# Performance work log

Measured on AMD Instinct MI355X. Metric: run time of the kernel, lower is better.

Reference implementation:

```python
import jax, jax.numpy as jnp
import numpy as np

B, W, CBLK, C, H, L, VOCAB = 8, 512, 24, 512, 8, 2, 256
HD = C // H


def _ln(x, g, b, eps=1e-5):
    m = x.mean(-1, keepdims=True)
    v = ((x - m) ** 2).mean(-1, keepdims=True)
    return (x - m) * jax.lax.rsqrt(v + eps) * g + b


def _causal_attn(q, k, v):
    # q,k,v: [..., T, hd]; causal softmax attention, scale 1/sqrt(hd)
    T = q.shape[-2]
    scale = 1.0 / (q.shape[-1] ** 0.5)
    s = jnp.einsum('...qd,...kd->...qk', q, k) * scale
    mask = jnp.tril(jnp.ones((T, T), dtype=bool))
    s = jnp.where(mask, s, jnp.finfo(s.dtype).min)
    return jnp.einsum('...qk,...kd->...qd', jax.nn.softmax(s, axis=-1), v)


def _mha_char(seq, w_qkv, last_ix):
    # seq: [B,W,c,C]; per-word causal char attention, then gather row last_ix
    b, w, c, _ = seq.shape
    q, k, v = jnp.split(seq @ w_qkv, 3, axis=-1)
    sh = lambda t: t.reshape(b, w, c, H, HD).transpose(0, 1, 3, 2, 4)
    o = _causal_attn(sh(q), sh(k), sh(v))          # [B,W,H,c,hd]
    o = o.transpose(0, 1, 3, 2, 4).reshape(b, w, c, C)
    return jnp.take_along_axis(o, last_ix[:, :, None, None], axis=2)[:, :, 0, :]


def _mha_word(x, w_qkv, w_proj):
    b, w, _ = x.shape
    q, k, v = jnp.split(x @ w_qkv, 3, axis=-1)
    sh = lambda t: t.reshape(b, w, H, HD).transpose(0, 2, 1, 3)
    o = _causal_attn(sh(q), sh(k), sh(v))
    o = o.transpose(0, 2, 1, 3).reshape(b, w, C)
    return o @ w_proj


def setup_inputs() -> dict:
    key = jax.random.key(0)
    ks = jax.random.split(key, 16)
    # ragged word lengths in [1, CBLK]; mask = ones then zeros (as produced by pad())
    lengths = jax.random.randint(ks[0], (B, W), 1, CBLK + 1)
    attention_mask = (jnp.arange(CBLK)[None, None, :] < lengths[:, :, None]).astype(jnp.int32)
    x = jax.random.randint(ks[1], (B, W, CBLK), 0, VOCAB).astype(jnp.int32)
    std = 0.02
    res_std = std * (2 * L) ** -0.5  # res_flag init scaling
    n = lambda k, s, sd=std: sd * jax.random.normal(k, s, dtype=jnp.float32)
    return dict(
        x=x, attention_mask=attention_mask,
        cte=n(ks[2], (VOCAB, C)), cpe=n(ks[3], (CBLK, C)), wpe=n(ks[4], (W, C)),
        ln1_g=jnp.ones((L, C)), ln1_b=jnp.zeros((L, C)),
        ln2_g=jnp.ones((L, C)), ln2_b=jnp.zeros((L, C)),
        ln3_g=jnp.ones((L, C)), ln3_b=jnp.zeros((L, C)),
        cattn_w=n(ks[5], (L, C, 3 * C)), cattn_proj=n(ks[6], (L, C, C)),
        wattn_w=n(ks[7], (L, C, 3 * C)), wattn_proj=n(ks[8], (L, C, C), res_std),
        mlp_fc=n(ks[9], (L, C, 4 * C)), mlp_proj=n(ks[10], (L, 4 * C, C), res_std),
        proj_w=n(ks[11], (C, CBLK * C)), lm_head_w=n(ks[12], (C, VOCAB)),
    )


def reference(x, attention_mask, cte, cpe, wpe, ln1_g, ln1_b, ln2_g, ln2_b, ln3_g, ln3_b,
              cattn_w, cattn_proj, wattn_w, wattn_proj, mlp_fc, mlp_proj, proj_w, lm_head_w):
    last_ix = attention_mask.sum(axis=2) - 1           # [B,W], last real char per word
    state = cte[x] + cpe[None, None, :, :]             # [B,W,c,C]
    context = None                                     # current_conv.context/pad, vectorized
    for l in range(L):
        if l == 0:
            # first_time: operate on full padded char sequences, cache ln_1 output
            hln = _ln(state, ln1_g[l], ln1_b[l])       # [B,W,c,C]
            context = hln
            seq = hln
        else:
            # splice the new word vector into position last_ix of the cached context
            hln = _ln(state, ln1_g[l], ln1_b[l])       # [B,W,C]
            repl = jnp.arange(CBLK)[None, None, :] == last_ix[:, :, None]
            seq = jnp.where(repl[..., None], hln[:, :, None, :], context)
        o = _mha_char(seq, cattn_w[l], last_ix)        # [B,W,C]
        if l == 0:
            o = o + wpe[None, :, :]                    # word pos emb added only first_time
        state = o @ cattn_proj[l]                      # note: no residual around c_attn
        state = state + _mha_word(_ln(state, ln2_g[l], ln2_b[l]), wattn_w[l], wattn_proj[l])
        hm = _ln(state, ln3_g[l], ln3_b[l])
        state = state + jax.nn.gelu(hm @ mlp_fc[l], approximate=False) @ mlp_proj[l]
    y = (state @ proj_w).reshape(B, W, CBLK, C)
    return y @ lm_head_w                               # logits [B,W,CBLK,VOCAB]
```

## Files before the change

kernel.cpp:

```cpp
#include <hip/hip_runtime.h>
#include <hip/hip_bf16.h>
#include <math.h>


namespace {

constexpr int Bn = 8, Wn = 512, CB = 24, Cd = 512, Hn = 8, Lln = 2, Vn = 256, HDn = 64;
constexpr int BW = Bn * Wn;
constexpr int C3 = 3 * Cd;
constexpr int FF = 4 * Cd;
constexpr int NROW = BW * CB;

typedef unsigned short u16;
typedef short short8 __attribute__((ext_vector_type(8)));
typedef float f32x4 __attribute__((ext_vector_type(4)));
typedef __attribute__((address_space(1))) void gvoid_t;
typedef __attribute__((address_space(3))) void lvoid_t;

__device__ __forceinline__ u16 f2bu(float f) {
  __hip_bfloat16 h = __float2bfloat16(f);
  return __builtin_bit_cast(u16, h);
}
__device__ __forceinline__ float bu2f(u16 u) {
  return __bfloat162float(__builtin_bit_cast(__hip_bfloat16, u));
}
__device__ __forceinline__ float geluf(float x) {
  return 0.5f * x * (1.0f + erff(x * 0.7071067811865475f));
}
__device__ __forceinline__ void gl16(const void* g, void* l) {
  __builtin_amdgcn_global_load_lds((gvoid_t*)g, (lvoid_t*)l, 16, 0, 0);
}

__global__ void k_lastix(const int* __restrict__ mask, int* __restrict__ lastix) {
  int i = blockIdx.x * 256 + threadIdx.x;
  if (i < BW) {
    int s = 0;
#pragma unroll
    for (int j = 0; j < CB; ++j) s += mask[i * CB + j];
    lastix[i] = s - 1;
  }
}

__device__ __forceinline__ void f2b8(const float* __restrict__ s, u16* __restrict__ d) {
  float4 a = *(const float4*)s;
  float4 b = *(const float4*)(s + 4);
  union { uint4 u; u16 h[8]; } pk;
  pk.h[0] = f2bu(a.x); pk.h[1] = f2bu(a.y); pk.h[2] = f2bu(a.z); pk.h[3] = f2bu(a.w);
  pk.h[4] = f2bu(b.x); pk.h[5] = f2bu(b.y); pk.h[6] = f2bu(b.z); pk.h[7] = f2bu(b.w);
  *(uint4*)d = pk.u;
}

__device__ __forceinline__ void wT_tile(const float* __restrict__ src, u16* __restrict__ dst,
                                        int K, int N, int n0, int k0,
                                        u16 T[64][72], int tid) {
  int kl = tid >> 2, nc = (tid & 3) * 16;
  const float* s = src + (long)(k0 + kl) * N + n0 + nc;
#pragma unroll
  for (int u = 0; u < 4; ++u) {
    float4 f = *(const float4*)(s + u * 4);
    T[nc + u * 4 + 0][kl] = f2bu(f.x);
    T[nc + u * 4 + 1][kl] = f2bu(f.y);
    T[nc + u * 4 + 2][kl] = f2bu(f.z);
    T[nc + u * 4 + 3][kl] = f2bu(f.w);
  }
  __syncthreads();
  int nl = tid >> 2, kc = (tid & 3) * 16;
  u16* d = dst + (long)(n0 + nl) * K + k0 + kc;
  *(uint4*)d = *(uint4*)&T[nl][kc];
  *(uint4*)(d + 8) = *(uint4*)&T[nl][kc + 8];
}

__global__ __launch_bounds__(256) void k_prep(
    const float* __restrict__ proj_w, u16* __restrict__ projwb,
    const float* __restrict__ cattn_w, u16* __restrict__ wcb,
    const float* __restrict__ lm_head, u16* __restrict__ lmhT,
    const float* __restrict__ cattn_proj, const float* __restrict__ wattn_w,
    const float* __restrict__ wattn_proj, const float* __restrict__ mlp_fc,
    const float* __restrict__ mlp_proj, u16* __restrict__ wT) {
  __shared__ u16 T[64][72];
  int b = blockIdx.x, tid = threadIdx.x;
  if (b < 3072) { long i = ((long)b * 256 + tid) * 8; f2b8(proj_w + i, projwb + i); return; }
  b -= 3072;
  if (b < 768) { long i = ((long)b * 256 + tid) * 8; f2b8(cattn_w + i, wcb + i); return; }
  b -= 768;
  if (b < 32) { wT_tile(lm_head, lmhT, Cd, Vn, (b & 3) * 64, (b >> 2) * 64, T, tid); return; }
  b -= 32;
  int l = b >> 10, r = b & 1023;
  size_t lw = (size_t)(2 * C3 * Cd + 2 * Cd * Cd + 2 * FF * Cd);
  u16* bl = wT + l * lw;
  const float* src; u16* dst; int K, N, nt;
  if (r < 192)      { src = cattn_w + (size_t)l * Cd * C3;    dst = bl;                              K = Cd; N = C3; nt = 24; }
  else if (r < 256) { src = cattn_proj + (size_t)l * Cd * Cd; dst = bl + C3 * Cd;                    K = Cd; N = Cd; nt = 8;  r -= 192; }
  else if (r < 448) { src = wattn_w + (size_t)l * Cd * C3;    dst = bl + C3 * Cd + Cd * Cd;          K = Cd; N = C3; nt = 24; r -= 256; }
  else if (r < 512) { src = wattn_proj + (size_t)l * Cd * Cd; dst = bl + 2 * C3 * Cd + Cd * Cd;      K = Cd; N = Cd; nt = 8;  r -= 448; }
  else if (r < 768) { src = mlp_fc + (size_t)l * Cd * FF;     dst = bl + 2 * C3 * Cd + 2 * Cd * Cd;  K = Cd; N = FF; nt = 32; r -= 512; }
  else              { src = mlp_proj + (size_t)l * FF * Cd;   dst = bl + 2 * C3 * Cd + 2 * Cd * Cd + FF * Cd; K = FF; N = Cd; nt = 8; r -= 768; }
  wT_tile(src, dst, K, N, (r % nt) * 64, (r / nt) * 64, T, tid);
}

__global__ __launch_bounds__(64) void k_embed_ln(
    const int* __restrict__ x, const float* __restrict__ cte, const float* __restrict__ cpe,
    const float* __restrict__ g, const float* __restrict__ b,
    const int* __restrict__ lastix, u16* __restrict__ ctx, u16* __restrict__ qin) {
  int r = blockIdx.x;
  int bw = r / CB, ch = r - bw * CB;
  int li = lastix[bw];
  if (ch > li) return;
  int tok = x[r];
  const float* e = cte + (long)tok * Cd;
  const float* pe = cpe + (long)ch * Cd;
  int lane = threadIdx.x;
  float v[8];
  float s = 0.f, sq = 0.f;
#pragma unroll
  for (int u = 0; u < 2; ++u) {
    float4 a = *(const float4*)(e + u * 256 + lane * 4);
    float4 p4 = *(const float4*)(pe + u * 256 + lane * 4);
    v[u * 4 + 0] = a.x + p4.x; v[u * 4 + 1] = a.y + p4.y;
    v[u * 4 + 2] = a.z + p4.z; v[u * 4 + 3] = a.w + p4.w;
  }
#pragma unroll
  for (int u = 0; u < 8; ++u) { s += v[u]; sq += v[u] * v[u]; }
#pragma unroll
  for (int m = 32; m; m >>= 1) { s += __shfl_xor(s, m); sq += __shfl_xor(sq, m); }
  float mean = s * (1.0f / Cd);
  float var = sq * (1.0f / Cd) - mean * mean;
  float rs = rsqrtf(var + 1e-5f);
  u16* o = ctx + (long)r * Cd;
  u16* oq = qin + (long)bw * Cd;
  int isLast = (ch == li);
#pragma unroll
  for (int u = 0; u < 2; ++u) {
    int c0 = u * 256 + lane * 4;
    float4 g4 = *(const float4*)(g + c0);
    float4 b4 = *(const float4*)(b + c0);
    float o0 = (v[u * 4 + 0] - mean) * rs * g4.x + b4.x;
    float o1 = (v[u * 4 + 1] - mean) * rs * g4.y + b4.y;
    float o2 = (v[u * 4 + 2] - mean) * rs * g4.z + b4.z;
    float o3 = (v[u * 4 + 3] - mean) * rs * g4.w + b4.w;
    uint2 w;
    w.x = (unsigned)f2bu(o0) | ((unsigned)f2bu(o1) << 16);
    w.y = (unsigned)f2bu(o2) | ((unsigned)f2bu(o3) << 16);
    *(uint2*)(o + c0) = w;
    if (isLast) *(uint2*)(oq + c0) = w;
  }
}

__global__ __launch_bounds__(64) void k_ln(
    const float* __restrict__ X, u16* __restrict__ Y,
    const float* __restrict__ g, const float* __restrict__ b) {
  long r = blockIdx.x;
  const float* xr = X + r * Cd;
  int lane = threadIdx.x;
  float v[8];
  float s = 0.f, sq = 0.f;
#pragma unroll
  for (int u = 0; u < 2; ++u) {
    float4 a = *(const float4*)(xr + u * 256 + lane * 4);
    v[u * 4 + 0] = a.x; v[u * 4 + 1] = a.y; v[u * 4 + 2] = a.z; v[u * 4 + 3] = a.w;
  }
#pragma unroll
  for (int u = 0; u < 8; ++u) { s += v[u]; sq += v[u] * v[u]; }
#pragma unroll
  for (int m = 32; m; m >>= 1) { s += __shfl_xor(s, m); sq += __shfl_xor(sq, m); }
  float mean = s * (1.0f / Cd);
  float var = sq * (1.0f / Cd) - mean * mean;
  float rs = rsqrtf(var + 1e-5f);
  u16* o = Y + r * Cd;
#pragma unroll
  for (int u = 0; u < 2; ++u) {
    int c0 = u * 256 + lane * 4;
    float4 g4 = *(const float4*)(g + c0);
    float4 b4 = *(const float4*)(b + c0);
    float o0 = (v[u * 4 + 0] - mean) * rs * g4.x + b4.x;
    float o1 = (v[u * 4 + 1] - mean) * rs * g4.y + b4.y;
    float o2 = (v[u * 4 + 2] - mean) * rs * g4.z + b4.z;
    float o3 = (v[u * 4 + 3] - mean) * rs * g4.w + b4.w;
    uint2 w;
    w.x = (unsigned)f2bu(o0) | ((unsigned)f2bu(o1) << 16);
    w.y = (unsigned)f2bu(o2) | ((unsigned)f2bu(o3) << 16);
    *(uint2*)(o + c0) = w;
  }
}

template <int BM, int BN, int EPI, int OUTBF>
__global__ __launch_bounds__(256) void k_mgemm(
    const u16* __restrict__ A, int lda, long sA1, long sA2,
    const u16* __restrict__ Bt, int ldb, long sB1, long sB2,
    void* __restrict__ Cv, int ldc, long sC1, long sC2,
    const float* __restrict__ R, u16* __restrict__ D2,
    const float* __restrict__ PL, const u16* __restrict__ VL,
    const float* __restrict__ WP, int K, int zdiv) {
  constexpr int WM = BM / 2;
  constexpr int WN = BN / 2;
  constexpr int FM = WM / 16, FN = WN / 16;
  __shared__ u16 As[BM * 32];
  __shared__ u16 Bs[BN * 32];
  long m0 = (long)blockIdx.y * BM, n0 = (long)blockIdx.x * BN;
  int z = blockIdx.z;
  int z1 = z / zdiv, z2 = z - z1 * zdiv;
  A += z1 * sA1 + z2 * sA2;
  Bt += z1 * sB1 + z2 * sB2;
  long coff = z1 * sC1 + z2 * sC2;
  int tid = threadIdx.x;
  int wid = tid >> 6, lane = tid & 63;
  int wr = wid >> 1, wc = wid & 1;

  const int srow = tid >> 2, skk = (tid & 3) * 8;
  const u16* Ald[BM / 64];
  const u16* Bld[BN / 64];
#pragma unroll
  for (int i = 0; i < BM / 64; ++i) Ald[i] = A + (m0 + srow + i * 64) * (long)lda + skk;
#pragma unroll
  for (int i = 0; i < BN / 64; ++i) Bld[i] = Bt + (n0 + srow + i * 64) * (long)ldb + skk;

  f32x4 acc[FM][FN] = {};
  const int fr = lane & 15, kg = lane >> 4;

  for (int k0 = 0; k0 < K; k0 += 32) {
#pragma unroll
    for (int i = 0; i < BM / 64; ++i) gl16(Ald[i] + k0, &As[(tid + i * 256) * 8]);
#pragma unroll
    for (int i = 0; i < BN / 64; ++i) gl16(Bld[i] + k0, &Bs[(tid + i * 256) * 8]);
    __syncthreads();
    short8 af[FM], bf[FN];
#pragma unroll
    for (int m = 0; m < FM; ++m)
      af[m] = *(const short8*)&As[(wr * WM + m * 16 + fr) * 32 + kg * 8];
#pragma unroll
    for (int n = 0; n < FN; ++n)
      bf[n] = *(const short8*)&Bs[(wc * WN + n * 16 + fr) * 32 + kg * 8];
#pragma unroll
    for (int m = 0; m < FM; ++m)
#pragma unroll
      for (int n = 0; n < FN; ++n)
        acc[m][n] = __builtin_amdgcn_mfma_f32_16x16x32_bf16(af[m], bf[n], acc[m][n], 0, 0, 0);
    __syncthreads();
  }
  int ccol = lane & 15, crow4 = (lane >> 4) * 4;
#pragma unroll
  for (int m = 0; m < FM; ++m)
#pragma unroll
    for (int n = 0; n < FN; ++n)
#pragma unroll
      for (int q = 0; q < 4; ++q) {
        long gr = m0 + wr * WM + m * 16 + crow4 + q;
        long gc = n0 + wc * WN + n * 16 + ccol;
        float v = acc[m][n][q];
        long idx = gr * (long)ldc + gc + coff;
        if (EPI == 1 || EPI == 3) v += R[idx];
        if (EPI == 2) v = geluf(v);
        if (EPI == 4) {
          v += PL[gr * 8 + z2] * bu2f(VL[gr * (long)C3 + 2 * Cd + z2 * 64 + gc]);
          if (WP) v += WP[(long)(gr & (Wn - 1)) * Cd + z2 * 64 + gc];
        }
        if (EPI == 3) {
          ((float*)Cv)[idx] = v;
          D2[idx] = f2bu(v);
        } else if (OUTBF) {
          ((u16*)Cv)[idx] = f2bu(v);
        } else {
          ((float*)Cv)[idx] = v;
        }
      }
}

__global__ __launch_bounds__(256) void k_cattn2(
    const u16* __restrict__ ctx, const u16* __restrict__ qtil,
    const u16* __restrict__ qkvc, const int* __restrict__ lastix,
    u16* __restrict__ U, float* __restrict__ plast) {
  constexpr int CS = 520;
  int gw = blockIdx.x;
  int li = lastix[gw];
  __shared__ u16 ctxs[CB - 1][CS];
  __shared__ float spf[4][Hn][32];
  __shared__ float sp[Hn][CB];
  int tid = threadIdx.x;
  for (int u = tid; u < li * 64; u += 256) {
    int row = u >> 6, c = (u & 63) * 8;
    *(uint4*)&ctxs[row][c] = *(const uint4*)(ctx + ((long)(gw * CB + row)) * Cd + c);
  }
  __syncthreads();
  int w = tid >> 6, lane = tid & 63;
  int fr = lane & 15, kg = lane >> 4;
  {
    const u16* qbase = qtil + (long)gw * 4096 + (fr & 7) * 512 + w * 128 + kg * 8;
    int r0 = fr;
    int r1 = 16 + fr; if (r1 > CB - 2) r1 = CB - 2;
    f32x4 acc0 = {}, acc1 = {};
#pragma unroll
    for (int kk = 0; kk < 4; ++kk) {
      short8 af = *(const short8*)(qbase + kk * 32);
      short8 b0 = *(const short8*)&ctxs[r0][w * 128 + kk * 32 + kg * 8];
      short8 b1 = *(const short8*)&ctxs[r1][w * 128 + kk * 32 + kg * 8];
      acc0 = __builtin_amdgcn_mfma_f32_16x16x32_bf16(af, b0, acc0, 0, 0, 0);
      acc1 = __builtin_amdgcn_mfma_f32_16x16x32_bf16(af, b1, acc1, 0, 0, 0);
    }
    if (lane < 32) {
      int jj = lane & 15;
#pragma unroll
      for (int q = 0; q < 4; ++q) {
        int h = (lane >> 4) * 4 + q;
        spf[w][h][jj] = acc0[q];
        spf[w][h][16 + jj] = acc1[q];
      }
    }
  }
  __syncthreads();
  {
    int h = tid >> 5, j = tid & 31;
    if (j < CB)
      sp[h][j] = (spf[0][h][j] + spf[1][h][j] + spf[2][h][j] + spf[3][h][j]) * 0.125f;
  }
  __syncthreads();
  if (tid < 8) {
    const u16* qq = qkvc + (long)gw * C3 + tid * 64;
    const u16* kk = qq + Cd;
    float s = 0.f;
#pragma unroll
    for (int u = 0; u < 64; ++u) s += bu2f(qq[u]) * bu2f(kk[u]);
    sp[tid][li] = s * 0.125f;
  }
  __syncthreads();
  if (tid < 8) {
    float m = -3.4e38f;
    for (int jj = 0; jj <= li; ++jj) m = fmaxf(m, sp[tid][jj]);
    float s = 0.f;
    for (int jj = 0; jj <= li; ++jj) { float e = expf(sp[tid][jj] - m); sp[tid][jj] = e; s += e; }
    float inv = 1.0f / s;
    for (int jj = 0; jj <= li; ++jj) sp[tid][jj] *= inv;
    plast[gw * 8 + tid] = sp[tid][li];
  }
  __syncthreads();
  int h = tid >> 5, d0 = (tid & 31) * 16;
  float uacc[16];
#pragma unroll
  for (int i = 0; i < 16; ++i) uacc[i] = 0.f;
  for (int jj = 0; jj < li; ++jj) {
    float p = sp[h][jj];
    const u16* cv = &ctxs[jj][d0];
#pragma unroll
    for (int i = 0; i < 16; ++i) uacc[i] += p * bu2f(cv[i]);
  }
  union { uint4 q[2]; u16 hh[16]; } pk;
#pragma unroll
  for (int i = 0; i < 16; ++i) pk.hh[i] = f2bu(uacc[i]);
  u16* d = U + (long)gw * 4096 + h * 512 + d0;
  *(uint4*)d = pk.q[0];
  *(uint4*)(d + 8) = pk.q[1];
}

__global__ __launch_bounds__(256) void k_fattn(
    const u16* __restrict__ qkv, u16* __restrict__ ao) {
  constexpr int ST = 68;
  __shared__ u16 Ks[64 * ST];
  __shared__ u16 Vs[64 * ST];
  __shared__ u16 Ps[4][16 * ST];
  int qt = blockIdx.x;
  int z  = blockIdx.y;
  int b = z >> 3, h = z & 7;
  int tid = threadIdx.x;
  int w = tid >> 6, lane = tid & 63;
  int fr = lane & 15, kg = lane >> 4;

  short8 qf[2];
  {
    const u16* qp = qkv + ((long)(b * Wn + qt * 64 + w * 16 + fr)) * C3 + h * 64 + kg * 8;
    qf[0] = *(const short8*)qp;
    qf[1] = *(const short8*)(qp + 32);
  }
  f32x4 oacc[4] = {};
  float mrow[4], lrow[4];
#pragma unroll
  for (int q = 0; q < 4; ++q) { mrow[q] = -3.4e38f; lrow[q] = 0.f; }

  for (int kt = 0; kt <= qt; ++kt) {
    __syncthreads();
    {
      int r = tid >> 2, c = (tid & 3) * 16;
      const u16* kp = qkv + ((long)(b * Wn + kt * 64 + r)) * C3 + Cd + h * 64 + c;
      *(uint4*)&Ks[r * ST + c] = *(const uint4*)kp;
      *(uint4*)&Ks[r * ST + c + 8] = *(const uint4*)(kp + 8);
      const u16* vp = kp + Cd;
      uint4 v0 = *(const uint4*)vp;
      uint4 v1 = *(const uint4*)(vp + 8);
      const u16* e0 = (const u16*)&v0;
      const u16* e1 = (const u16*)&v1;
#pragma unroll
      for (int u = 0; u < 8; ++u) Vs[(c + u) * ST + r] = e0[u];
#pragma unroll
      for (int u = 0; u < 8; ++u) Vs[(c + 8 + u) * ST + r] = e1[u];
    }
    __syncthreads();
    f32x4 s[4];
#pragma unroll
    for (int n = 0; n < 4; ++n) {
      short8 kf0 = *(const short8*)&Ks[(n * 16 + fr) * ST + kg * 8];
      short8 kf1 = *(const short8*)&Ks[(n * 16 + fr) * ST + kg * 8 + 32];
      f32x4 a = {};
      a = __builtin_amdgcn_mfma_f32_16x16x32_bf16(qf[0], kf0, a, 0, 0, 0);
      a = __builtin_amdgcn_mfma_f32_16x16x32_bf16(qf[1], kf1, a, 0, 0, 0);
      s[n] = a;
    }
    int irow0 = qt * 64 + w * 16 + kg * 4;
#pragma unroll
    for (int n = 0; n < 4; ++n) {
      int jcol = kt * 64 + n * 16 + fr;
#pragma unroll
      for (int q = 0; q < 4; ++q) {
        float v = s[n][q] * 0.125f;
        s[n][q] = (jcol > irow0 + q) ? -3.4e38f : v;
      }
    }
    float sf[4];
#pragma unroll
    for (int q = 0; q < 4; ++q) {
      float mm = fmaxf(fmaxf(s[0][q], s[1][q]), fmaxf(s[2][q], s[3][q]));
      mm = fmaxf(mm, __shfl_xor(mm, 1));
      mm = fmaxf(mm, __shfl_xor(mm, 2));
      mm = fmaxf(mm, __shfl_xor(mm, 4));
      mm = fmaxf(mm, __shfl_xor(mm, 8));
      float mnew = fmaxf(mrow[q], mm);
      sf[q] = expf(mrow[q] - mnew);
      mrow[q] = mnew;
    }
    float ls[4] = {0.f, 0.f, 0.f, 0.f};
#pragma unroll
    for (int n = 0; n < 4; ++n) {
#pragma unroll
      for (int q = 0; q < 4; ++q) {
        float p = expf(s[n][q] - mrow[q]);
        u16 pb = f2bu(p);
        ls[q] += bu2f(pb);
        Ps[w][(kg * 4 + q) * ST + n * 16 + fr] = pb;
      }
    }
#pragma unroll
    for (int q = 0; q < 4; ++q) {
      float l = ls[q];
      l += __shfl_xor(l, 1); l += __shfl_xor(l, 2);
      l += __shfl_xor(l, 4); l += __shfl_xor(l, 8);
      lrow[q] = lrow[q] * sf[q] + l;
#pragma unroll
      for (int n = 0; n < 4; ++n) oacc[n][q] *= sf[q];
    }
    asm volatile("s_waitcnt lgkmcnt(0)" ::: "memory");
    short8 pa0 = *(const short8*)&Ps[w][fr * ST + kg * 8];
    short8 pa1 = *(const short8*)&Ps[w][fr * ST + kg * 8 + 32];
#pragma unroll
    for (int n = 0; n < 4; ++n) {
      short8 vf0 = *(const short8*)&Vs[(n * 16 + fr) * ST + kg * 8];
      short8 vf1 = *(const short8*)&Vs[(n * 16 + fr) * ST + kg * 8 + 32];
      oacc[n] = __builtin_amdgcn_mfma_f32_16x16x32_bf16(pa0, vf0, oacc[n], 0, 0, 0);
      oacc[n] = __builtin_amdgcn_mfma_f32_16x16x32_bf16(pa1, vf1, oacc[n], 0, 0, 0);
    }
  }
  int orow = b * Wn + qt * 64 + w * 16 + kg * 4;
#pragma unroll
  for (int q = 0; q < 4; ++q) {
    float inv = 1.0f / lrow[q];
#pragma unroll
    for (int n = 0; n < 4; ++n)
      ao[(long)(orow + q) * Cd + h * 64 + n * 16 + fr] = f2bu(oacc[n][q] * inv);
  }
}

template <int BM, int BN, int EPI, int OUTBF>
static inline void mgemm(hipStream_t st,
    const u16* A, int lda, long sA1, long sA2,
    const u16* Bt, int ldb, long sB1, long sB2,
    void* C, int ldc, long sC1, long sC2,
    const float* R, int M, int N, int K, int nz, int zdiv,
    u16* D2 = nullptr, const float* PL = nullptr, const u16* VL = nullptr,
    const float* WP = nullptr) {
  dim3 g(N / BN, (M + BM - 1) / BM, nz);
  hipLaunchKernelGGL((k_mgemm<BM, BN, EPI, OUTBF>), g, dim3(256), 0, st,
                     A, lda, sA1, sA2, Bt, ldb, sB1, sB2, C, ldc, sC1, sC2,
                     R ? R : (const float*)C, D2, PL, VL, WP, K, zdiv);
}

}

extern "C" void kernel_launch(void* const* d_in, const int* in_sizes, int n_in,
                              void* d_out, int out_size, void* d_ws, size_t ws_size,
                              hipStream_t stream) {
  (void)in_sizes; (void)n_in; (void)out_size; (void)ws_size;
  const int*   x          = (const int*)d_in[0];
  const int*   amask      = (const int*)d_in[1];
  const float* cte        = (const float*)d_in[2];
  const float* cpe        = (const float*)d_in[3];
  const float* wpe        = (const float*)d_in[4];
  const float* ln1g       = (const float*)d_in[5];
  const float* ln1b       = (const float*)d_in[6];
  const float* ln2g       = (const float*)d_in[7];
  const float* ln2b       = (const float*)d_in[8];
  const float* ln3g       = (const float*)d_in[9];
  const float* ln3b       = (const float*)d_in[10];
  const float* cattn_w    = (const float*)d_in[11];
  const float* cattn_proj = (const float*)d_in[12];
  const float* wattn_w    = (const float*)d_in[13];
  const float* wattn_proj = (const float*)d_in[14];
  const float* mlp_fc     = (const float*)d_in[15];
  const float* mlp_proj   = (const float*)d_in[16];
  const float* proj_w     = (const float*)d_in[17];
  const float* lm_head    = (const float*)d_in[18];
  float* out = (float*)d_out;

  char* base = (char*)d_ws;
  size_t off = 0;
  auto alloc = [&](size_t bytes) -> char* {
    char* r = base + off;
    off += (bytes + 255) & ~(size_t)255;
    return r;
  };
  int*   lastix = (int*)alloc((size_t)BW * 4);
  float* plast  = (float*)alloc((size_t)BW * 8 * 4);
  u16*   ctx    = (u16*)alloc((size_t)NROW * Cd * 2);
  char*  big    = alloc((size_t)105 * 1024 * 1024);
  u16*   kvq    = (u16*)alloc((size_t)BW * C3 * 2);
  u16*   qin    = (u16*)alloc((size_t)BW * Cd * 2);
  float* state  = (float*)alloc((size_t)BW * Cd * 4);
  u16*   stateb = (u16*)alloc((size_t)BW * Cd * 2);
  u16*   hln    = (u16*)alloc((size_t)BW * Cd * 2);
  u16*   ao     = (u16*)alloc((size_t)BW * Cd * 2);
  u16*   wT     = (u16*)alloc((size_t)2 * (2 * C3 * Cd + 2 * Cd * Cd + 2 * FF * Cd) * 2);
  u16*   wcb    = (u16*)alloc((size_t)2 * Cd * C3 * 2);
  u16*   projwb = (u16*)alloc((size_t)Cd * CB * Cd * 2);
  u16*   lmhT   = (u16*)alloc((size_t)Vn * Cd * 2);

  u16*   U     = (u16*)big;
  u16*   qtil  = (u16*)(big + (size_t)35651584);
  u16*   mlph  = (u16*)big;
  u16*   combT = (u16*)big;

  size_t lw = (size_t)(2 * C3 * Cd + 2 * Cd * Cd + 2 * FF * Cd);
  auto cwT    = [&](int l) { return wT + l * lw; };
  auto cprojT = [&](int l) { return wT + l * lw + C3 * Cd; };
  auto wwT    = [&](int l) { return wT + l * lw + C3 * Cd + Cd * Cd; };
  auto wprojT = [&](int l) { return wT + l * lw + 2 * C3 * Cd + Cd * Cd; };
  auto fcT    = [&](int l) { return wT + l * lw + 2 * C3 * Cd + 2 * Cd * Cd; };
  auto mprojT = [&](int l) { return wT + l * lw + 2 * C3 * Cd + 2 * Cd * Cd + FF * Cd; };

  hipLaunchKernelGGL(k_lastix, dim3(16), dim3(256), 0, stream, amask, lastix);
  hipLaunchKernelGGL(k_prep, dim3(5920), dim3(256), 0, stream,
                     proj_w, projwb, cattn_w, wcb, lm_head, lmhT,
                     cattn_proj, wattn_w, wattn_proj, mlp_fc, mlp_proj, wT);
  hipLaunchKernelGGL(k_embed_ln, dim3(NROW), dim3(64), 0, stream,
                     x, cte, cpe, ln1g, ln1b, lastix, ctx, qin);

  for (int l = 0; l < Lln; ++l) {
    u16* qkvc = kvq;
    u16* qkvw = kvq;
    if (l > 0)
      hipLaunchKernelGGL(k_ln, dim3(BW), dim3(64), 0, stream, state, qin, ln1g + Cd, ln1b + Cd);
    mgemm<128, 64, 0, 1>(stream, qin, Cd, 0, 0, cwT(l), Cd, 0, 0,
                         qkvc, C3, 0, 0, nullptr, BW, C3, Cd, 1, 1);
    mgemm<64, 64, 0, 1>(stream, qkvc, C3, 0, 64,
                        wcb + (size_t)l * Cd * C3 + Cd, C3, 0, 64,
                        qtil, 8 * Cd, 0, Cd, nullptr, BW, Cd, HDn, 8, 8);
    hipLaunchKernelGGL(k_cattn2, dim3(BW), dim3(256), 0, stream,
                       ctx, qtil, qkvc, lastix, U, plast);
    mgemm<64, 64, 4, 1>(stream, U, 8 * Cd, 0, Cd,
                        cwT(l) + (size_t)(2 * Cd) * Cd, Cd, 0, (long)HDn * Cd,
                        ao, Cd, 0, HDn, nullptr, BW, HDn, Cd, 8, 8,
                        nullptr, plast, qkvc, l == 0 ? wpe : nullptr);
    mgemm<64, 64, 0, 0>(stream, ao, Cd, 0, 0, cprojT(l), Cd, 0, 0,
                        state, Cd, 0, 0, nullptr, BW, Cd, Cd, 1, 1);
    hipLaunchKernelGGL(k_ln, dim3(BW), dim3(64), 0, stream, state, hln, ln2g + l * Cd, ln2b + l * Cd);
    mgemm<128, 64, 0, 1>(stream, hln, Cd, 0, 0, wwT(l), Cd, 0, 0,
                         qkvw, C3, 0, 0, nullptr, BW, C3, Cd, 1, 1);
    hipLaunchKernelGGL(k_fattn, dim3(8, 64), dim3(256), 0, stream, qkvw, ao);
    mgemm<64, 64, 1, 0>(stream, ao, Cd, 0, 0, wprojT(l), Cd, 0, 0,
                        state, Cd, 0, 0, state, BW, Cd, Cd, 1, 1);
    hipLaunchKernelGGL(k_ln, dim3(BW), dim3(64), 0, stream, state, hln, ln3g + l * Cd, ln3b + l * Cd);
    mgemm<64, 64, 2, 1>(stream, hln, Cd, 0, 0, fcT(l), Cd, 0, 0,
                        mlph, FF, 0, 0, nullptr, BW, FF, Cd, 1, 1);
    mgemm<64, 64, 3, 0>(stream, mlph, FF, 0, 0, mprojT(l), FF, 0, 0,
                        state, Cd, 0, 0, state, BW, Cd, FF, 1, 1, stateb);
  }

  mgemm<64, 64, 0, 1>(stream, lmhT, Cd, 0, 0,
                      projwb, CB * Cd, 0, Cd,
                      combT, Cd, 0, (long)Vn * Cd,
                      nullptr, Vn, Cd, Cd, CB, CB);
  mgemm<128, 128, 0, 0>(stream, stateb, Cd, 0, 0, combT, Cd, 0, 0,
                        out, CB * Vn, 0, 0, nullptr, BW, CB * Vn, Cd, 1, 1);
}
```

Measured before the change: 539.1 us.

## Use MFMA for char-attention P·V and fold lastix into prep kernel

The weighted sum of cached context rows in the char attention kernel now runs as a bf16 MFMA. Probabilities are packed as bf16 into a small shared tile and the unused context rows are zero-padded, replacing the per-thread scalar FMA loop over up to 23 rows. Separately, the last-index computation is merged into the weight-prep launch as extra blocks, removing one kernel launch. The trade-off is that probabilities are rounded to bf16 before the product, and the gathered B fragments use strided shared-memory reads that may cause bank conflicts.

```diff
diff --git a/kernel.cpp b/kernel.cpp
--- a/kernel.cpp
+++ b/kernel.cpp
@@ -29,16 +29,6 @@
 }
 __device__ __forceinline__ void gl16(const void* g, void* l) {
   __builtin_amdgcn_global_load_lds((gvoid_t*)g, (lvoid_t*)l, 16, 0, 0);
-}
-
-__global__ void k_lastix(const int* __restrict__ mask, int* __restrict__ lastix) {
-  int i = blockIdx.x * 256 + threadIdx.x;
-  if (i < BW) {
-    int s = 0;
-#pragma unroll
-    for (int j = 0; j < CB; ++j) s += mask[i * CB + j];
-    lastix[i] = s - 1;
-  }
 }
 
 __device__ __forceinline__ void f2b8(const float* __restrict__ s, u16* __restrict__ d) {
@@ -76,9 +66,20 @@
     const float* __restrict__ lm_head, u16* __restrict__ lmhT,
     const float* __restrict__ cattn_proj, const float* __restrict__ wattn_w,
     const float* __restrict__ wattn_proj, const float* __restrict__ mlp_fc,
-    const float* __restrict__ mlp_proj, u16* __restrict__ wT) {
+    const float* __restrict__ mlp_proj, u16* __restrict__ wT,
+    const int* __restrict__ amask, int* __restrict__ lastix) {
   __shared__ u16 T[64][72];
   int b = blockIdx.x, tid = threadIdx.x;
+  if (b >= 5920) {
+    int i = (b - 5920) * 256 + tid;
+    if (i < BW) {
+      int s = 0;
+#pragma unroll
+      for (int j = 0; j < CB; ++j) s += amask[i * CB + j];
+      lastix[i] = s - 1;
+    }
+    return;
+  }
   if (b < 3072) { long i = ((long)b * 256 + tid) * 8; f2b8(proj_w + i, projwb + i); return; }
   b -= 3072;
   if (b < 768) { long i = ((long)b * 256 + tid) * 8; f2b8(cattn_w + i, wcb + i); return; }
@@ -275,10 +276,15 @@
   __shared__ u16 ctxs[CB - 1][CS];
   __shared__ float spf[4][Hn][32];
   __shared__ float sp[Hn][CB];
+  __shared__ u16 Pb[16][40];
   int tid = threadIdx.x;
   for (int u = tid; u < li * 64; u += 256) {
     int row = u >> 6, c = (u & 63) * 8;
     *(uint4*)&ctxs[row][c] = *(const uint4*)(ctx + ((long)(gw * CB + row)) * Cd + c);
+  }
+  for (int u = tid; u < (CB - 1 - li) * 64; u += 256) {
+    int row = li + (u >> 6), c = (u & 63) * 8;
+    *(uint4*)&ctxs[row][c] = make_uint4(0, 0, 0, 0);
   }
   __syncthreads();
   int w = tid >> 6, lane = tid & 63;
@@ -312,6 +318,7 @@
     if (j < CB)
       sp[h][j] = (spf[0][h][j] + spf[1][h][j] + spf[2][h][j] + spf[3][h][j]) * 0.125f;
   }
+  for (int u = tid; u < 16 * 40; u += 256) ((u16*)Pb)[u] = 0;
   __syncthreads();
   if (tid < 8) {
     const u16* qq = qkvc + (long)gw * C3 + tid * 64;
@@ -328,26 +335,32 @@
     float s = 0.f;
     for (int jj = 0; jj <= li; ++jj) { float e = expf(sp[tid][jj] - m); sp[tid][jj] = e; s += e; }
     float inv = 1.0f / s;
-    for (int jj = 0; jj <= li; ++jj) sp[tid][jj] *= inv;
-    plast[gw * 8 + tid] = sp[tid][li];
+    for (int jj = 0; jj < li; ++jj) Pb[tid][jj] = f2bu(sp[tid][jj] * inv);
+    plast[gw * 8 + tid] = sp[tid][li] * inv;
   }
   __syncthreads();
-  int h = tid >> 5, d0 = (tid & 31) * 16;
-  float uacc[16];
-#pragma unroll
-  for (int i = 0; i < 16; ++i) uacc[i] = 0.f;
-  for (int jj = 0; jj < li; ++jj) {
-    float p = sp[h][jj];
-    const u16* cv = &ctxs[jj][d0];
-#pragma unroll
-    for (int i = 0; i < 16; ++i) uacc[i] += p * bu2f(cv[i]);
-  }
-  union { uint4 q[2]; u16 hh[16]; } pk;
-#pragma unroll
-  for (int i = 0; i < 16; ++i) pk.hh[i] = f2bu(uacc[i]);
-  u16* d = U + (long)gw * 4096 + h * 512 + d0;
-  *(uint4*)d = pk.q[0];
-  *(uint4*)(d + 8) = pk.q[1];
+  {
+    short8 pf = *(const short8*)&Pb[fr][kg * 8];
+    u16* ub = U + (long)gw * 4096;
+#pragma unroll
+    for (int t = 0; t < 8; ++t) {
+      int n0 = (w * 8 + t) * 16;
+      union { short8 v; u16 e[8]; } bf;
+#pragma unroll
+      for (int u = 0; u < 8; ++u) {
+        int k = kg * 8 + u;
+        int kc = k < CB - 1 ? k : CB - 2;
+        bf.e[u] = ctxs[kc][n0 + fr];
+      }
+      f32x4 a = {};
+      a = __builtin_amdgcn_mfma_f32_16x16x32_bf16(pf, bf.v, a, 0, 0, 0);
+      if (kg < 2) {
+#pragma unroll
+        for (int q = 0; q < 4; ++q)
+          ub[(kg * 4 + q) * 512 + n0 + fr] = f2bu(a[q]);
+      }
+    }
+  }
 }
 
 __global__ __launch_bounds__(256) void k_fattn(
@@ -541,10 +554,10 @@
   auto fcT    = [&](int l) { return wT + l * lw + 2 * C3 * Cd + 2 * Cd * Cd; };
   auto mprojT = [&](int l) { return wT + l * lw + 2 * C3 * Cd + 2 * Cd * Cd + FF * Cd; };
 
-  hipLaunchKernelGGL(k_lastix, dim3(16), dim3(256), 0, stream, amask, lastix);
-  hipLaunchKernelGGL(k_prep, dim3(5920), dim3(256), 0, stream,
+  hipLaunchKernelGGL(k_prep, dim3(5936), dim3(256), 0, stream,
                      proj_w, projwb, cattn_w, wcb, lm_head, lmhT,
-                     cattn_proj, wattn_w, wattn_proj, mlp_fc, mlp_proj, wT);
+                     cattn_proj, wattn_w, wattn_proj, mlp_fc, mlp_proj, wT,
+                     amask, lastix);
   hipLaunchKernelGGL(k_embed_ln, dim3(NROW), dim3(64), 0, stream,
                      x, cte, cpe, ln1g, ln1b, lastix, ctx, qin);
 
```

Result: faster. 527.8 us (median of 2 runs) (-2.1%).
